# Performance work log

Measured on AMD Instinct MI355X. Metric: run time of the kernel, lower is better.

The kernel has to match this reference:

```python
import jax, jax.numpy as jnp
import numpy as np

H = 16  # n_heads
EPS = 1e-12  # torch F.normalize eps


def setup_inputs() -> dict:
    key = jax.random.key(0)
    ks = jax.random.split(key, 7)
    dim = 1024
    b, n = 8, 4096
    s = 1.0 / np.sqrt(dim)
    return {
        "x": jax.random.normal(ks[0], (b, n, dim), dtype=jnp.float32),
        "Wq": jax.random.normal(ks[1], (dim, dim), dtype=jnp.float32) * s,
        "Wk": jax.random.normal(ks[2], (dim, dim), dtype=jnp.float32) * s,
        "Wv": jax.random.normal(ks[3], (dim, dim), dtype=jnp.float32) * s,
        "scale": jnp.ones((H, 1, 1), dtype=jnp.float32),
        "Wo": jax.random.normal(ks[4], (dim, dim), dtype=jnp.float32) * s,
        "bo": jnp.zeros((dim,), dtype=jnp.float32),
    }


def _l2norm(t):
    # F.normalize(t, dim=-1, p=2): t / max(||t||_2, eps)
    nrm = jnp.sqrt(jnp.sum(t * t, axis=-1, keepdims=True))
    return t / jnp.maximum(nrm, EPS)


def reference(x, Wq, Wk, Wv, scale, Wo, bo):
    b, n, c = x.shape
    d = c // H

    def proj_t(W):
        # Linear (x @ W.T) -> [b, n, h, d] -> transposed layout [b, h, d, n]
        return (x @ W.T).reshape(b, n, H, d).transpose(0, 2, 3, 1)

    q = _l2norm(proj_t(Wq))  # [b, h, d, n], L2-normalized over tokens
    k = _l2norm(proj_t(Wk))
    v = proj_t(Wv)

    # cross-covariance attention over channel dim: [b, h, d, d]
    attn = jnp.einsum('bhdn,bhen->bhde', k, q) * scale
    attn = jax.nn.softmax(attn, axis=-1)
    out = jnp.einsum('bhde,bhen->bhdn', attn, v)  # [b, h, d, n]

    # faithful to torch: raw view of contiguous [b, h, d, n] into [b, n, c]
    out = out.reshape(b, n, c)
    return out @ Wo.T + bo
```

## Files before the change

### kernel.cpp

```cpp
#include <hip/hip_runtime.h>
#include <stdint.h>


typedef unsigned short u16;
typedef __attribute__((ext_vector_type(8))) short bf16x8;
typedef __attribute__((ext_vector_type(8))) u16 u16x8;
typedef __attribute__((ext_vector_type(4))) u16 u16x4;
typedef __attribute__((ext_vector_type(4))) float f32x4;

__device__ __forceinline__ float bf2f(u16 u) {
  union { unsigned int i; float f; } x;
  x.i = ((unsigned int)u) << 16;
  return x.f;
}
__device__ __forceinline__ u16 f2bf(float f) {
  union { float f; unsigned int i; } x;
  x.f = f;
  unsigned int u = x.i;
  u = u + 0x7fffu + ((u >> 16) & 1u);
  return (u16)(u >> 16);
}

__device__ __forceinline__ void gload16(const u16* g, u16* l) {
  __builtin_amdgcn_global_load_lds(
      (const __attribute__((address_space(1))) void*)g,
      (__attribute__((address_space(3))) void*)l, 16, 0, 0);
}

__global__ __launch_bounds__(256) void cast_kernel(
    const float4* __restrict__ x, const float4* __restrict__ wq,
    const float4* __restrict__ wk, const float4* __restrict__ wv,
    const float4* __restrict__ wo, u16x4* __restrict__ xbf,
    u16x4* __restrict__ wbf) {
  long i = (long)blockIdx.x * 256 + threadIdx.x;
  float4 v = x[i];
  u16x4 o;
  o[0] = f2bf(v.x); o[1] = f2bf(v.y); o[2] = f2bf(v.z); o[3] = f2bf(v.w);
  xbf[i] = o;
  if (i < 1048576) {
    int sel = (int)(i >> 18);
    const float4* s = (sel == 0) ? wq : (sel == 1) ? wk : (sel == 2) ? wv : wo;
    float4 w = s[i & 262143];
    u16x4 ow;
    ow[0] = f2bf(w.x); ow[1] = f2bf(w.y); ow[2] = f2bf(w.z); ow[3] = f2bf(w.w);
    wbf[i] = ow;
  }
}


#define STG(Lb, G, r0, kt)                                                   \
  gload16((G) + (long)((r0) + rl) * 1024 + (kt) * 64 + slswz,                \
          (Lb) + (r0) * 64 + tid * 8)

#define BRD(Bb, ksel)                                                        \
  _Pragma("unroll") for (int jj = 0; jj < 4; ++jj) {                         \
    const int idx = (wc * 64 + jj * 16 + fm) * 64 + (ksel)*32 + fk;          \
    bfr[jj][ksel] = *(const bf16x8*)((Bb) + (idx ^ swz));                    \
  }

#define ARD(Ab, qr, ksel)                                                    \
  _Pragma("unroll") for (int i = 0; i < 4; ++i) {                            \
    const int idx = (wr * 128 + (qr)*64 + i * 16 + fm) * 64 + (ksel)*32 + fk;\
    aC[i] = *(const bf16x8*)((Ab) + (idx ^ swz));                            \
  }

#define MM16(qr, ksel)                                                       \
  {                                                                          \
    __builtin_amdgcn_s_setprio(1);                                           \
    _Pragma("unroll") for (int i = 0; i < 4; ++i)                            \
    _Pragma("unroll") for (int j = 0; j < 4; ++j)                            \
        acc[(qr)*4 + i][j] = __builtin_amdgcn_mfma_f32_16x16x32_bf16(        \
            aC[i], bfr[j][ksel], acc[(qr)*4 + i][j], 0, 0, 0);               \
    __builtin_amdgcn_s_setprio(0);                                           \
  }

#define LGKM0 asm volatile("s_waitcnt lgkmcnt(0)" ::: "memory")
#define VM4 asm volatile("s_waitcnt vmcnt(4)" ::: "memory")
#define VM0 asm volatile("s_waitcnt vmcnt(0)" ::: "memory")
#define VMNONE (void)0
#define BAR __builtin_amdgcn_s_barrier()
#define SCB __builtin_amdgcn_sched_barrier(0)

#define TILE(Ab, Bb, Aoth, kt, SA, SB, VMW)                                  \
  {                                                                          \
                                                                     \
    BRD(Bb, 0); ARD(Ab, 0, 0);                                               \
    if (SA) { STG(Aoth, Ag, 128, (kt) + 1); STG(Aoth, Ag, 192, (kt) + 1); }  \
    SCB; BAR; LGKM0; SCB;                                                    \
    MM16(0, 0); BAR;                                                         \
                                                                     \
    BRD(Bb, 1); ARD(Ab, 0, 1);                                               \
    if (SA) { STG(Aoth, Ag, 0, (kt) + 1); STG(Aoth, Ag, 64, (kt) + 1); }     \
    SCB; BAR; LGKM0; SCB;                                                    \
    MM16(0, 1); BAR;                                                         \
                                                                     \
    ARD(Ab, 1, 0);                                                           \
    if (SB) { STG(Bb, Bg, 0, (kt) + 2); STG(Bb, Bg, 64, (kt) + 2); }         \
    SCB; BAR; LGKM0; SCB;                                                    \
    MM16(1, 0); BAR;                                                         \
                                                                     \
    ARD(Ab, 1, 1);                                                           \
    if (SB) { STG(Bb, Bg, 128, (kt) + 2); STG(Bb, Bg, 192, (kt) + 2); }      \
    SCB; BAR; LGKM0; SCB;                                                    \
    MM16(1, 1); VMW; BAR;                                                    \
  }

template <int MODE>
__global__ __launch_bounds__(512, 2) void gemm256(const u16* __restrict__ A,
                                                  const u16* __restrict__ B,
                                                  void* __restrict__ C,
                                                  const float* __restrict__ bias) {
  __shared__ u16 As0[16384];
  __shared__ u16 As1[16384];
  __shared__ u16 Bs0[16384];
  __shared__ u16 Bs1[16384];
  const int tid = threadIdx.x;
  const int lane = tid & 63;
  const int wave = tid >> 6;
  const int wr = wave >> 2;
  const int wc = wave & 3;
  const int m0 = blockIdx.y * 256;
  const int n0 = blockIdx.x * 256;

  long aoff, boff, coff;
  if (MODE == 0) {
    int w = blockIdx.z >> 3;
    int b = blockIdx.z & 7;
    aoff = (long)w * 1048576;
    boff = (long)b * 4194304;
    coff = (long)blockIdx.z * 4194304;
  } else {
    aoff = (long)blockIdx.z * 4194304;
    boff = 0;
    coff = (long)blockIdx.z * 4194304;
  }
  const u16* Ag = A + aoff + (long)m0 * 1024;
  const u16* Bg = B + boff + (long)n0 * 1024;

  const int rl = tid >> 3;
  const int slswz = ((tid & 7) ^ (rl & 7)) * 8;
  const int fm = lane & 15;
  const int fk = (lane >> 4) << 3;
  const int swz = (fm & 7) << 3;

  f32x4 acc[8][4];
  const f32x4 z4 = {0.f, 0.f, 0.f, 0.f};
#pragma unroll
  for (int i = 0; i < 8; i++)
#pragma unroll
    for (int j = 0; j < 4; j++) acc[i][j] = z4;

  bf16x8 aC[4], bfr[4][2];

  STG(Bs0, Bg, 0, 0);   STG(Bs0, Bg, 64, 0);
  STG(Bs0, Bg, 128, 0); STG(Bs0, Bg, 192, 0);
  STG(As0, Ag, 128, 0); STG(As0, Ag, 192, 0);
  STG(As0, Ag, 0, 0);   STG(As0, Ag, 64, 0);
  STG(Bs1, Bg, 0, 1);   STG(Bs1, Bg, 64, 1);
  STG(Bs1, Bg, 128, 1); STG(Bs1, Bg, 192, 1);
  VM4;
  BAR;

#pragma unroll 1
  for (int it = 0; it < 7; ++it) {
    TILE(As0, Bs0, As1, 2 * it, true, true, VM4);
    TILE(As1, Bs1, As0, 2 * it + 1, true, true, VM4);
  }
  TILE(As0, Bs0, As1, 14, true, false, VM0);
  TILE(As1, Bs1, As0, 15, false, false, VMNONE);

  const int rq = (lane >> 4) * 4;
  const int mBase = m0 + wr * 128;
  const int nBase = n0 + wc * 64;
  if (MODE == 1) {
    float* Cf = (float*)C + coff;
#pragma unroll
    for (int jj = 0; jj < 4; ++jj) {
      float bv = bias[nBase + jj * 16 + fm];
#pragma unroll
      for (int i = 0; i < 8; ++i)
#pragma unroll
        for (int r = 0; r < 4; ++r) {
          int m = mBase + i * 16 + rq + r;
          int n = nBase + jj * 16 + fm;
          Cf[(long)m * 1024 + n] = acc[i][jj][r] + bv;
        }
    }
  } else {
    const int ldc = (MODE == 0) ? 4096 : 1024;
    u16* Cb = (u16*)C + coff;
#pragma unroll
    for (int i = 0; i < 8; ++i)
#pragma unroll
      for (int jj = 0; jj < 4; ++jj)
#pragma unroll
        for (int r = 0; r < 4; ++r) {
          int m = mBase + i * 16 + rq + r;
          int n = nBase + jj * 16 + fm;
          Cb[(long)m * ldc + n] = f2bf(acc[i][jj][r]);
        }
  }
}

__global__ __launch_bounds__(256) void attn_partial(const u16* __restrict__ qk,
                                                    float* __restrict__ attnP,
                                                    float* __restrict__ nsqP) {
  const int bh = blockIdx.x;
  const int b = bh >> 4, h = bh & 15;
  const int tid = threadIdx.x, lane = tid & 63, wave = tid >> 6;
  const int sl = blockIdx.y * 4 + wave;
  const u16* Qg = qk + (long)b * 4194304 + (long)h * 64 * 4096;
  const u16* Kg = Qg + 33554432L;

  const int fm = lane & 15;
  const long kbase = (long)sl * 256 + (lane >> 4) * 8;

  f32x4 acc[4][4];
  const f32x4 z4 = {0.f, 0.f, 0.f, 0.f};
#pragma unroll
  for (int i = 0; i < 4; i++)
#pragma unroll
    for (int j = 0; j < 4; j++) acc[i][j] = z4;
  float sk[4] = {0.f, 0.f, 0.f, 0.f}, sq[4] = {0.f, 0.f, 0.f, 0.f};

  for (int kt = 0; kt < 256; kt += 32) {
    bf16x8 ak[4], aq[4];
#pragma unroll
    for (int i = 0; i < 4; i++) {
      ak[i] = *(const bf16x8*)(Kg + (long)(i * 16 + fm) * 4096 + kbase + kt);
      aq[i] = *(const bf16x8*)(Qg + (long)(i * 16 + fm) * 4096 + kbase + kt);
    }
#pragma unroll
    for (int i = 0; i < 4; i++) {
      const u16x8 kv = (u16x8)ak[i], qv = (u16x8)aq[i];
#pragma unroll
      for (int e = 0; e < 8; e++) {
        float fkk = bf2f(kv[e]); sk[i] += fkk * fkk;
        float fq = bf2f(qv[e]);  sq[i] += fq * fq;
      }
    }
#pragma unroll
    for (int i = 0; i < 4; i++)
#pragma unroll
      for (int j = 0; j < 4; j++)
        acc[i][j] = __builtin_amdgcn_mfma_f32_16x16x32_bf16(ak[i], aq[j],
                                                            acc[i][j], 0, 0, 0);
  }

#pragma unroll
  for (int i = 0; i < 4; i++) {
    sk[i] += __shfl_xor(sk[i], 16); sk[i] += __shfl_xor(sk[i], 32);
    sq[i] += __shfl_xor(sq[i], 16); sq[i] += __shfl_xor(sq[i], 32);
  }
  float* np = nsqP + ((long)sl * 128 + bh) * 128;
  if (lane < 16) {
#pragma unroll
    for (int i = 0; i < 4; i++) {
      np[i * 16 + lane] = sk[i];
      np[64 + i * 16 + lane] = sq[i];
    }
  }
  float* sp = attnP + ((long)sl * 128 + bh) * 4096;
  const int rq = (lane >> 4) * 4;
#pragma unroll
  for (int i = 0; i < 4; i++)
#pragma unroll
    for (int j = 0; j < 4; j++)
#pragma unroll
      for (int r = 0; r < 4; r++)
        sp[(i * 16 + rq + r) * 64 + j * 16 + fm] = acc[i][j][r];
}

__global__ __launch_bounds__(256) void attn_finalize(const float* __restrict__ attnP,
                                                     const float* __restrict__ nsqP,
                                                     const float* __restrict__ scale,
                                                     u16* __restrict__ attnb) {
  const int bh = blockIdx.x;
  const int dz = blockIdx.y;
  const int h = bh & 15;
  const int tid = threadIdx.x;
  __shared__ float rn[2][64];
  if (tid < 128) {
    int which = tid >> 6, row = tid & 63;
    float s = 0.f;
#pragma unroll
    for (int sl = 0; sl < 16; sl++)
      s += nsqP[((long)sl * 128 + bh) * 128 + which * 64 + row];
    rn[which][row] = 1.0f / fmaxf(sqrtf(s), 1e-12f);
  }
  __syncthreads();
  const int d = dz * 32 + (tid >> 3);
  const int ec = tid & 7;
  float row[8];
#pragma unroll
  for (int e = 0; e < 8; e++) row[e] = 0.f;
  for (int sl = 0; sl < 16; sl++) {
    const float4* p = (const float4*)(attnP + ((long)sl * 128 + bh) * 4096 +
                                      d * 64 + ec * 8);
    float4 v0 = p[0], v1 = p[1];
    row[0] += v0.x; row[1] += v0.y; row[2] += v0.z; row[3] += v0.w;
    row[4] += v1.x; row[5] += v1.y; row[6] += v1.z; row[7] += v1.w;
  }
  const float rk = rn[0][d] * scale[h];
  float mx = -1e30f;
#pragma unroll
  for (int e = 0; e < 8; e++) {
    row[e] = row[e] * rk * rn[1][ec * 8 + e];
    mx = fmaxf(mx, row[e]);
  }
  mx = fmaxf(mx, __shfl_xor(mx, 1));
  mx = fmaxf(mx, __shfl_xor(mx, 2));
  mx = fmaxf(mx, __shfl_xor(mx, 4));
  float sum = 0.f;
#pragma unroll
  for (int e = 0; e < 8; e++) {
    row[e] = __expf(row[e] - mx);
    sum += row[e];
  }
  sum += __shfl_xor(sum, 1);
  sum += __shfl_xor(sum, 2);
  sum += __shfl_xor(sum, 4);
  float inv = 1.0f / sum;
  u16x8 o;
#pragma unroll
  for (int e = 0; e < 8; e++) o[e] = f2bf(row[e] * inv);
  *(u16x8*)(attnb + (long)bh * 4096 + d * 64 + ec * 8) = o;
}

__global__ __launch_bounds__(256) void av_mfma(const u16* __restrict__ attnb,
                                               const u16* __restrict__ vt,
                                               u16* __restrict__ outb) {
  const int bh = blockIdx.y;
  const int b = bh >> 4, h = bh & 15;
  const int n0 = blockIdx.x * 256;
  const int tid = threadIdx.x, lane = tid & 63, wave = tid >> 6;
  __shared__ u16 As[64 * 72];
  {
    const u16* src = attnb + (long)bh * 4096 + (tid >> 2) * 64 + (tid & 3) * 16;
    u16x8 v0 = *(const u16x8*)src;
    u16x8 v1 = *(const u16x8*)(src + 8);
    u16* dst = As + (tid >> 2) * 72 + (tid & 3) * 16;
    *(u16x8*)dst = v0;
    *(u16x8*)(dst + 8) = v1;
  }
  __syncthreads();
  const int fm = lane & 15;
  const int fe = (lane >> 4) * 8;
  const u16* Vg = vt + (long)b * 4194304 + h * 64 + fe;

  f32x4 acc[4][4];
  const f32x4 z4 = {0.f, 0.f, 0.f, 0.f};
#pragma unroll
  for (int i = 0; i < 4; i++)
#pragma unroll
    for (int j = 0; j < 4; j++) acc[i][j] = z4;

  bf16x8 af[4][2];
#pragma unroll
  for (int i = 0; i < 4; i++)
#pragma unroll
    for (int ks = 0; ks < 2; ks++)
      af[i][ks] = *(const bf16x8*)&As[(i * 16 + fm) * 72 + fe + ks * 32];

#pragma unroll
  for (int ks = 0; ks < 2; ks++)
#pragma unroll
    for (int j = 0; j < 4; j++) {
      int n = n0 + wave * 64 + j * 16 + fm;
      bf16x8 bf = *(const bf16x8*)(Vg + (long)n * 1024 + ks * 32);
#pragma unroll
      for (int i = 0; i < 4; i++)
        acc[i][j] = __builtin_amdgcn_mfma_f32_16x16x32_bf16(af[i][ks], bf,
                                                            acc[i][j], 0, 0, 0);
    }

  const int rq = (lane >> 4) * 4;
  u16* Ob = outb + ((long)b * 1024 + h * 64) * 4096;
#pragma unroll
  for (int i = 0; i < 4; i++)
#pragma unroll
    for (int j = 0; j < 4; j++)
#pragma unroll
      for (int r = 0; r < 4; r++) {
        int d = i * 16 + rq + r;
        int n = n0 + wave * 64 + j * 16 + fm;
        Ob[(long)d * 4096 + n] = f2bf(acc[i][j][r]);
      }
}

extern "C" void kernel_launch(void* const* d_in, const int* in_sizes, int n_in,
                              void* d_out, int out_size, void* d_ws, size_t ws_size,
                              hipStream_t stream) {
  const float* x = (const float*)d_in[0];
  const float* Wq = (const float*)d_in[1];
  const float* Wk = (const float*)d_in[2];
  const float* Wv = (const float*)d_in[3];
  const float* scale = (const float*)d_in[4];
  const float* Wo = (const float*)d_in[5];
  const float* bo = (const float*)d_in[6];
  float* out = (float*)d_out;

  u16* xbf = (u16*)d_ws;
  u16* wbf = xbf + 33554432;
  u16* qk = wbf + 4194304;
  u16* vt = qk + 67108864;
  float* attnP = (float*)(vt + 33554432);
  float* nsqP = attnP + 8388608;
  u16* attnb = (u16*)(nsqP + 262144);
  u16* outb = qk;

  cast_kernel<<<32768, 256, 0, stream>>>((const float4*)x, (const float4*)Wq,
                                         (const float4*)Wk, (const float4*)Wv,
                                         (const float4*)Wo, (u16x4*)xbf,
                                         (u16x4*)wbf);
  gemm256<0><<<dim3(16, 4, 16), 512, 0, stream>>>(wbf, xbf, (void*)qk, nullptr);
  gemm256<2><<<dim3(4, 16, 8), 512, 0, stream>>>(xbf, wbf + 2 * 1048576,
                                                 (void*)vt, nullptr);
  attn_partial<<<dim3(128, 4), 256, 0, stream>>>(qk, attnP, nsqP);
  attn_finalize<<<dim3(128, 2), 256, 0, stream>>>(attnP, nsqP, scale, attnb);
  av_mfma<<<dim3(16, 128), 256, 0, stream>>>(attnb, vt, outb);
  gemm256<1><<<dim3(4, 16, 8), 512, 0, stream>>>(outb, wbf + 3 * 1048576,
                                                 (void*)out, bo);
}
```

Before: 611.7 us.

## Double-buffer register fragments to overlap LDS reads with MFMA in GEMM

Restructures the GEMM main loop so the LDS fragment loads for the next quarter-step are issued before the MFMAs on the current fragments run, using two register fragment sets (a0f/a1f, b0f/b1f). The extra barrier before each MFMA group is removed, and the prologue now prefetches part of the next A tile along with the first fragments. This hides LDS read latency behind matrix work, but it raises register pressure and changes the global-load staging order and waitcnt accounting, which could be wrong or cause spills.

```diff
diff --git a/kernel.cpp b/kernel.cpp
--- a/kernel.cpp
+++ b/kernel.cpp
@@ -52,57 +52,54 @@
   gload16((G) + (long)((r0) + rl) * 1024 + (kt) * 64 + slswz,                \
           (Lb) + (r0) * 64 + tid * 8)
 
-#define BRD(Bb, ksel)                                                        \
+#define BRD(dst, Bb, ksel)                                                   \
   _Pragma("unroll") for (int jj = 0; jj < 4; ++jj) {                         \
     const int idx = (wc * 64 + jj * 16 + fm) * 64 + (ksel)*32 + fk;          \
-    bfr[jj][ksel] = *(const bf16x8*)((Bb) + (idx ^ swz));                    \
-  }
-
-#define ARD(Ab, qr, ksel)                                                    \
+    dst[jj] = *(const bf16x8*)((Bb) + (idx ^ swz));                          \
+  }
+
+#define ARD(dst, Ab, qr, ksel)                                               \
   _Pragma("unroll") for (int i = 0; i < 4; ++i) {                            \
     const int idx = (wr * 128 + (qr)*64 + i * 16 + fm) * 64 + (ksel)*32 + fk;\
-    aC[i] = *(const bf16x8*)((Ab) + (idx ^ swz));                            \
-  }
-
-#define MM16(qr, ksel)                                                       \
+    dst[i] = *(const bf16x8*)((Ab) + (idx ^ swz));                           \
+  }
+
+#define MMC(base, as, bs)                                                    \
   {                                                                          \
     __builtin_amdgcn_s_setprio(1);                                           \
     _Pragma("unroll") for (int i = 0; i < 4; ++i)                            \
     _Pragma("unroll") for (int j = 0; j < 4; ++j)                            \
-        acc[(qr)*4 + i][j] = __builtin_amdgcn_mfma_f32_16x16x32_bf16(        \
-            aC[i], bfr[j][ksel], acc[(qr)*4 + i][j], 0, 0, 0);               \
+        acc[(base) + i][j] = __builtin_amdgcn_mfma_f32_16x16x32_bf16(        \
+            as[i], bs[j], acc[(base) + i][j], 0, 0, 0);                      \
     __builtin_amdgcn_s_setprio(0);                                           \
   }
 
 #define LGKM0 asm volatile("s_waitcnt lgkmcnt(0)" ::: "memory")
 #define VM4 asm volatile("s_waitcnt vmcnt(4)" ::: "memory")
+#define VM6 asm volatile("s_waitcnt vmcnt(6)" ::: "memory")
 #define VM0 asm volatile("s_waitcnt vmcnt(0)" ::: "memory")
 #define VMNONE (void)0
 #define BAR __builtin_amdgcn_s_barrier()
 #define SCB __builtin_amdgcn_sched_barrier(0)
 
-#define TILE(Ab, Bb, Aoth, kt, SA, SB, VMW)                                  \
+#define TILE(cA, cB, nA, nB, kt, SA0, SB, SA3, RD3, VMW)                     \
   {                                                                          \
                                                                      \
-    BRD(Bb, 0); ARD(Ab, 0, 0);                                               \
-    if (SA) { STG(Aoth, Ag, 128, (kt) + 1); STG(Aoth, Ag, 192, (kt) + 1); }  \
-    SCB; BAR; LGKM0; SCB;                                                    \
-    MM16(0, 0); BAR;                                                         \
+    BRD(b1f, cB, 1); ARD(a1f, cA, 0, 1);                                     \
+    if (SA0) { STG(nA, Ag, 128, (kt) + 1); STG(nA, Ag, 192, (kt) + 1); }     \
+    MMC(0, a0f, b0f); SCB; LGKM0; BAR;                                       \
                                                                      \
-    BRD(Bb, 1); ARD(Ab, 0, 1);                                               \
-    if (SA) { STG(Aoth, Ag, 0, (kt) + 1); STG(Aoth, Ag, 64, (kt) + 1); }     \
-    SCB; BAR; LGKM0; SCB;                                                    \
-    MM16(0, 1); BAR;                                                         \
+    ARD(a0f, cA, 1, 0);                                                      \
+    if (SB) { STG(cB, Bg, 0, (kt) + 2); STG(cB, Bg, 64, (kt) + 2); }         \
+    MMC(0, a1f, b1f); SCB; LGKM0; BAR;                                       \
                                                                      \
-    ARD(Ab, 1, 0);                                                           \
-    if (SB) { STG(Bb, Bg, 0, (kt) + 2); STG(Bb, Bg, 64, (kt) + 2); }         \
-    SCB; BAR; LGKM0; SCB;                                                    \
-    MM16(1, 0); BAR;                                                         \
+    ARD(a1f, cA, 1, 1);                                                      \
+    if (SB) { STG(cB, Bg, 128, (kt) + 2); STG(cB, Bg, 192, (kt) + 2); }      \
+    MMC(4, a0f, b0f); SCB; LGKM0; VMW; BAR;                                  \
                                                                      \
-    ARD(Ab, 1, 1);                                                           \
-    if (SB) { STG(Bb, Bg, 128, (kt) + 2); STG(Bb, Bg, 192, (kt) + 2); }      \
-    SCB; BAR; LGKM0; SCB;                                                    \
-    MM16(1, 1); VMW; BAR;                                                    \
+    if (RD3) { BRD(b0f, nB, 0); ARD(a0f, nA, 0, 0); }                        \
+    if (SA3) { STG(cA, Ag, 0, (kt) + 2); STG(cA, Ag, 64, (kt) + 2); }        \
+    MMC(4, a1f, b1f); SCB; LGKM0; BAR;                                       \
   }
 
 template <int MODE>
@@ -150,24 +147,26 @@
 #pragma unroll
     for (int j = 0; j < 4; j++) acc[i][j] = z4;
 
-  bf16x8 aC[4], bfr[4][2];
+  bf16x8 a0f[4], a1f[4], b0f[4], b1f[4];
 
   STG(Bs0, Bg, 0, 0);   STG(Bs0, Bg, 64, 0);
   STG(Bs0, Bg, 128, 0); STG(Bs0, Bg, 192, 0);
+  STG(As0, Ag, 0, 0);   STG(As0, Ag, 64, 0);
   STG(As0, Ag, 128, 0); STG(As0, Ag, 192, 0);
-  STG(As0, Ag, 0, 0);   STG(As0, Ag, 64, 0);
   STG(Bs1, Bg, 0, 1);   STG(Bs1, Bg, 64, 1);
   STG(Bs1, Bg, 128, 1); STG(Bs1, Bg, 192, 1);
-  VM4;
+  STG(As1, Ag, 0, 1);   STG(As1, Ag, 64, 1);
+  VM6;
   BAR;
+  BRD(b0f, Bs0, 0); ARD(a0f, As0, 0, 0); LGKM0;
 
 #pragma unroll 1
   for (int it = 0; it < 7; ++it) {
-    TILE(As0, Bs0, As1, 2 * it, true, true, VM4);
-    TILE(As1, Bs1, As0, 2 * it + 1, true, true, VM4);
-  }
-  TILE(As0, Bs0, As1, 14, true, false, VM0);
-  TILE(As1, Bs1, As0, 15, false, false, VMNONE);
+    TILE(As0, Bs0, As1, Bs1, 2 * it, 1, 1, 1, 1, VM4);
+    TILE(As1, Bs1, As0, Bs0, 2 * it + 1, 1, 1, 1, 1, VM4);
+  }
+  TILE(As0, Bs0, As1, Bs1, 14, 1, 0, 0, 1, VM0);
+  TILE(As1, Bs1, As0, Bs0, 15, 0, 0, 0, 0, VMNONE);
 
   const int rq = (lane >> 4) * 4;
   const int mBase = m0 + wr * 128;
```

After: 648.5 us. 6.0% more time.
